# Kernel optimization log

Measured on AMD Instinct MI355X. Metric: run time of the kernel, lower is better.

## Reference

```python
import jax, jax.numpy as jnp
import numpy as np

ALPHA = 0.2  # LeakyReLU negative slope
N, F_IN, F_OUT = 8192, 512, 64
NEG_BIG = -9e15


def setup_inputs() -> dict:
    key = jax.random.key(0)
    k1, k2, k3, k4 = jax.random.split(key, 4)
    h = jax.random.normal(k1, (N, F_IN), dtype=jnp.float32)
    # xavier_uniform with gain 1.414
    lim_w = 1.414 * np.sqrt(6.0 / (F_IN + F_OUT))
    W = jax.random.uniform(k2, (F_IN, F_OUT), dtype=jnp.float32, minval=-lim_w, maxval=lim_w)
    lim_a = 1.414 * np.sqrt(6.0 / (2 * F_OUT + 1))
    a = jax.random.uniform(k3, (2 * F_OUT, 1), dtype=jnp.float32, minval=-lim_a, maxval=lim_a)
    adj = jax.random.randint(k4, (N, N), 0, 2, dtype=jnp.int32)
    return {"h": h, "W": W, "a": a, "adj": adj}


def reference(h, W, a, adj):
    Wh = h @ W                                  # [N, F_OUT]
    f_out = Wh.shape[1]
    a1 = a[:f_out, 0]                            # source half of attention vector
    a2 = a[f_out:, 0]                            # target half
    # e_ij = LeakyReLU(Wh_i . a1 + Wh_j . a2); equals cat([Wh_i, Wh_j]) @ a
    e = jax.nn.leaky_relu(jnp.matmul(Wh, a1)[:, None] + jnp.matmul(Wh, a2)[None, :], ALPHA)  # [N, N]
    attention = jnp.where(adj > 0, e, NEG_BIG)
    attention = jax.nn.softmax(attention, axis=1)
    # dropout is a no-op at inference (training=False)
    h_prime = attention @ Wh                     # [N, F_OUT]
    return jax.nn.elu(h_prime)                   # concat=True -> ELU
```

## Files before the change

### kernel.cpp

```cpp
#include <hip/hip_runtime.h>
#include <hip/hip_bf16.h>


typedef _Float16 f16;
typedef _Float16 f16x8 __attribute__((ext_vector_type(8)));
typedef float f32x4 __attribute__((ext_vector_type(4)));

#define GAT_N 8192
#define GAT_FIN 512
#define GAT_FOUT 64
#define GAT_ALPHA 0.2f

__global__ void k0_wtrans(const float* __restrict__ W, f16* __restrict__ WT) {
    int idx = blockIdx.x * blockDim.x + threadIdx.x;
    int k = idx >> 6, c = idx & 63;
    WT[c * GAT_FIN + k] = (f16)W[idx];
}

__global__ __launch_bounds__(64) void k1_gemm(const float* __restrict__ h,
        const f16* __restrict__ WT, const float* __restrict__ a,
        f16* __restrict__ WhT, float* __restrict__ s1, float* __restrict__ s2) {
    int lane = threadIdx.x & 63;
    int l15 = lane & 15, quad = lane >> 4;
    int rb = blockIdx.x * 16;
    size_t arow = (size_t)(rb + l15) * GAT_FIN;

    f32x4 acc[4] = {};
    for (int k0 = 0; k0 < GAT_FIN; k0 += 32) {
        int kb = k0 + quad * 8;
        const float4* hp = (const float4*)(h + arow + kb);
        float4 h0 = hp[0], h1 = hp[1];
        f16x8 af = { (f16)h0.x, (f16)h0.y, (f16)h0.z, (f16)h0.w,
                     (f16)h1.x, (f16)h1.y, (f16)h1.z, (f16)h1.w };
#pragma unroll
        for (int t = 0; t < 4; t++) {
            f16x8 bf = *(const f16x8*)(WT + (t * 16 + l15) * GAT_FIN + kb);
            acc[t] = __builtin_amdgcn_mfma_f32_16x16x32_f16(af, bf, acc[t], 0, 0, 0);
        }
    }

    float a1v[4], a2v[4];
#pragma unroll
    for (int t = 0; t < 4; t++) {
        a1v[t] = a[t * 16 + l15];
        a2v[t] = a[GAT_FOUT + t * 16 + l15];
    }
#pragma unroll
    for (int reg = 0; reg < 4; reg++) {
        int r = rb + quad * 4 + reg;
        float p1 = 0.f, p2 = 0.f;
#pragma unroll
        for (int t = 0; t < 4; t++) {
            float v = acc[t][reg];
            WhT[(size_t)(t * 16 + l15) * GAT_N + r] = (f16)v;
            p1 += v * a1v[t];
            p2 += v * a2v[t];
        }
#pragma unroll
        for (int off = 1; off < 16; off <<= 1) {
            p1 += __shfl_xor(p1, off);
            p2 += __shfl_xor(p2, off);
        }
        if (l15 == 0) { s1[r] = p1; s2[r] = p2; }
    }
}

__global__ void k2_max(const float* __restrict__ s2, float* __restrict__ mx) {
    __shared__ float red[256];
    float m = -1e30f;
    for (int i = threadIdx.x; i < GAT_N; i += 256) m = fmaxf(m, s2[i]);
    red[threadIdx.x] = m;
    __syncthreads();
    for (int s = 128; s > 0; s >>= 1) {
        if (threadIdx.x < s) red[threadIdx.x] = fmaxf(red[threadIdx.x], red[threadIdx.x + s]);
        __syncthreads();
    }
    if (threadIdx.x == 0) mx[0] = red[0];
}

__global__ __launch_bounds__(512) void k3_attn(const int* __restrict__ adj,
        const f16* __restrict__ WhT, const float* __restrict__ s1,
        const float* __restrict__ s2, const float* __restrict__ mxp,
        float* __restrict__ out) {
    __shared__ float accbuf[8][16][64];
    __shared__ float dbuf[8][16];

    int tid = threadIdx.x;
    int w = tid >> 6, lane = tid & 63;
    int l15 = lane & 15, quad = lane >> 4;
    int rb = blockIdx.x * 16;
    int row = rb + l15;

    float s1r = s1[row];
    float cr = s1r + mxp[0];
    cr = fmaxf(cr, GAT_ALPHA * cr);

    f32x4 acc[4] = {};
    float dacc = 0.f;
    const int* adjrow = adj + (size_t)row * GAT_N;

    for (int step = w; step < GAT_N / 32; step += 8) {
        int kb = step * 32 + quad * 8;
        int4 av0 = *(const int4*)(adjrow + kb);
        int4 av1 = *(const int4*)(adjrow + kb + 4);
        float4 sv0 = *(const float4*)(s2 + kb);
        float4 sv1 = *(const float4*)(s2 + kb + 4);

        int   am[8] = { av0.x, av0.y, av0.z, av0.w, av1.x, av1.y, av1.z, av1.w };
        float sv[8] = { sv0.x, sv0.y, sv0.z, sv0.w, sv1.x, sv1.y, sv1.z, sv1.w };

        f16x8 af;
#pragma unroll
        for (int j = 0; j < 8; j++) {
            float e = s1r + sv[j];
            e = fmaxf(e, GAT_ALPHA * e);
            float pf = __expf(e - cr);
            pf = (am[j] > 0) ? pf : 0.0f;
            dacc += pf;
            af[j] = (f16)pf;
        }
#pragma unroll
        for (int t = 0; t < 4; t++) {
            f16x8 bf = *(const f16x8*)(WhT + (size_t)(t * 16 + l15) * GAT_N + kb);
            acc[t] = __builtin_amdgcn_mfma_f32_16x16x32_f16(af, bf, acc[t], 0, 0, 0);
        }
    }

    dacc += __shfl_xor(dacc, 16);
    dacc += __shfl_xor(dacc, 32);

#pragma unroll
    for (int t = 0; t < 4; t++)
#pragma unroll
        for (int reg = 0; reg < 4; reg++)
            accbuf[w][quad * 4 + reg][t * 16 + l15] = acc[t][reg];
    if (quad == 0) dbuf[w][l15] = dacc;
    __syncthreads();

    for (int o = tid; o < 16 * 64; o += 512) {
        int r = o >> 6, c = o & 63;
        float num = 0.f, den = 0.f;
#pragma unroll
        for (int ww = 0; ww < 8; ww++) { num += accbuf[ww][r][c]; den += dbuf[ww][r]; }
        float hp = num / den;
        out[(size_t)(rb + r) * GAT_FOUT + c] = hp > 0.f ? hp : expm1f(hp);
    }
}

extern "C" void kernel_launch(void* const* d_in, const int* in_sizes, int n_in,
                              void* d_out, int out_size, void* d_ws, size_t ws_size,
                              hipStream_t stream) {
    const float* h   = (const float*)d_in[0];
    const float* W   = (const float*)d_in[1];
    const float* a   = (const float*)d_in[2];
    const int*   adj = (const int*)d_in[3];
    float* out = (float*)d_out;

    char* ws = (char*)d_ws;
    f16*   WT  = (f16*)ws;
    f16*   WhT = (f16*)(ws + 65536);
    float* s1  = (float*)(ws + 65536 + 1048576);
    float* s2  = (float*)(ws + 65536 + 1048576 + 32768);
    float* mx  = (float*)(ws + 65536 + 1048576 + 65536);

    k0_wtrans<<<128, 256, 0, stream>>>(W, WT);
    k1_gemm<<<512, 64, 0, stream>>>(h, WT, a, WhT, s1, s2);
    k2_max<<<1, 256, 0, stream>>>(s2, mx);
    k3_attn<<<512, 512, 0, stream>>>(adj, WhT, s1, s2, mx, out);
}
```

Before: 433.2 us.

## Coalesce adj row reads and stage softmax weights through double-buffered LDS

The attention kernel now assigns whole adjacency rows to half-waves, so each lane reads contiguous 16-byte chunks along a row instead of scattered 32-byte pieces across 16 rows. The exp and mask results are written into a double-buffered shared-memory tile in MFMA A-operand layout, then read back by each wave for the MFMA accumulation. Loads for the next 512-column chunk are issued before the current chunk's MFMAs to overlap the memory latency. This adds an LDS round trip and a block-wide barrier per chunk, and sets a minimum-blocks occupancy hint.

```diff
diff --git a/kernel.cpp b/kernel.cpp
--- a/kernel.cpp
+++ b/kernel.cpp
@@ -3,6 +3,7 @@
 
 
 typedef _Float16 f16;
+typedef _Float16 f16x2 __attribute__((ext_vector_type(2)));
 typedef _Float16 f16x8 __attribute__((ext_vector_type(8)));
 typedef float f32x4 __attribute__((ext_vector_type(4)));
 
@@ -78,72 +79,105 @@
     if (threadIdx.x == 0) mx[0] = red[0];
 }
 
-__global__ __launch_bounds__(512) void k3_attn(const int* __restrict__ adj,
+__global__ __launch_bounds__(512, 4) void k3_attn(const int* __restrict__ adj,
         const f16* __restrict__ WhT, const float* __restrict__ s1,
         const float* __restrict__ s2, const float* __restrict__ mxp,
         float* __restrict__ out) {
-    __shared__ float accbuf[8][16][64];
-    __shared__ float dbuf[8][16];
+    __shared__ __align__(16) char smem[2 * 16 * 520 * 2];
+    f16* pbuf = (f16*)smem;
+    float (*accbuf)[16][64] = (float (*)[16][64])smem;
+    __shared__ float dbuf2[16];
 
     int tid = threadIdx.x;
     int w = tid >> 6, lane = tid & 63;
     int l15 = lane & 15, quad = lane >> 4;
+    int hhalf = lane >> 5, q = lane & 31;
     int rb = blockIdx.x * 16;
-    int row = rb + l15;
-
-    float s1r = s1[row];
+    int r = 2 * w + hhalf;
+
+    float s1r = s1[rb + r];
     float cr = s1r + mxp[0];
     cr = fmaxf(cr, GAT_ALPHA * cr);
-
+    const int* adjrow = adj + (size_t)(rb + r) * GAT_N;
+
+    float dacc = 0.f;
     f32x4 acc[4] = {};
-    float dacc = 0.f;
-    const int* adjrow = adj + (size_t)row * GAT_N;
-
-    for (int step = w; step < GAT_N / 32; step += 8) {
-        int kb = step * 32 + quad * 8;
-        int4 av0 = *(const int4*)(adjrow + kb);
-        int4 av1 = *(const int4*)(adjrow + kb + 4);
-        float4 sv0 = *(const float4*)(s2 + kb);
-        float4 sv1 = *(const float4*)(s2 + kb + 4);
-
-        int   am[8] = { av0.x, av0.y, av0.z, av0.w, av1.x, av1.y, av1.z, av1.w };
-        float sv[8] = { sv0.x, sv0.y, sv0.z, sv0.w, sv1.x, sv1.y, sv1.z, sv1.w };
-
-        f16x8 af;
-#pragma unroll
-        for (int j = 0; j < 8; j++) {
-            float e = s1r + sv[j];
-            e = fmaxf(e, GAT_ALPHA * e);
-            float pf = __expf(e - cr);
-            pf = (am[j] > 0) ? pf : 0.0f;
-            dacc += pf;
-            af[j] = (f16)pf;
-        }
-#pragma unroll
-        for (int t = 0; t < 4; t++) {
-            f16x8 bf = *(const f16x8*)(WhT + (size_t)(t * 16 + l15) * GAT_N + kb);
-            acc[t] = __builtin_amdgcn_mfma_f32_16x16x32_f16(af, bf, acc[t], 0, 0, 0);
-        }
-    }
-
-    dacc += __shfl_xor(dacc, 16);
-    dacc += __shfl_xor(dacc, 32);
+    int4   av[4];
+    float4 sv[4];
+
+    auto stage = [&](int bb) {
+#pragma unroll
+        for (int p = 0; p < 4; p++) {
+            int   am[4]  = { av[p].x, av[p].y, av[p].z, av[p].w };
+            float svv[4] = { sv[p].x, sv[p].y, sv[p].z, sv[p].w };
+            int base = (4 * p + (q >> 3)) * 520 + ((q >> 1) & 3) * 128 + r * 8 + (q & 1) * 4;
+            f16 pf[4];
+#pragma unroll
+            for (int j = 0; j < 4; j++) {
+                float e = s1r + svv[j];
+                e = fmaxf(e, GAT_ALPHA * e);
+                float pv = __expf(e - cr);
+                pv = (am[j] > 0) ? pv : 0.0f;
+                dacc += pv;
+                pf[j] = (f16)pv;
+            }
+            f16x2 lo = { pf[0], pf[1] }, hi = { pf[2], pf[3] };
+            *(f16x2*)&pbuf[bb * 8320 + base]     = lo;
+            *(f16x2*)&pbuf[bb * 8320 + base + 2] = hi;
+        }
+    };
+
+#pragma unroll
+    for (int p = 0; p < 4; p++) {
+        int c0 = p * 128 + q * 4;
+        av[p] = *(const int4*)(adjrow + c0);
+        sv[p] = *(const float4*)(s2 + c0);
+    }
+    stage(0);
+    __syncthreads();
+
+    for (int rd = 0; rd < 16; rd++) {
+        int b = rd & 1;
+        if (rd < 15) {
+#pragma unroll
+            for (int p = 0; p < 4; p++) {
+                int c0 = (rd + 1) * 512 + p * 128 + q * 4;
+                av[p] = *(const int4*)(adjrow + c0);
+                sv[p] = *(const float4*)(s2 + c0);
+            }
+        }
+#pragma unroll
+        for (int sl = 0; sl < 2; sl++) {
+            int s_loc = 2 * w + sl;
+            f16x8 af = *(const f16x8*)&pbuf[b * 8320 + s_loc * 520 + lane * 8];
+            int kb = rd * 512 + s_loc * 32 + quad * 8;
+#pragma unroll
+            for (int t = 0; t < 4; t++) {
+                f16x8 bf = *(const f16x8*)(WhT + (size_t)(t * 16 + l15) * GAT_N + kb);
+                acc[t] = __builtin_amdgcn_mfma_f32_16x16x32_f16(af, bf, acc[t], 0, 0, 0);
+            }
+        }
+        if (rd < 15) stage(1 - b);
+        __syncthreads();
+    }
 
 #pragma unroll
     for (int t = 0; t < 4; t++)
 #pragma unroll
         for (int reg = 0; reg < 4; reg++)
             accbuf[w][quad * 4 + reg][t * 16 + l15] = acc[t][reg];
-    if (quad == 0) dbuf[w][l15] = dacc;
+#pragma unroll
+    for (int off = 16; off >= 1; off >>= 1) dacc += __shfl_xor(dacc, off);
+    if (q == 0) dbuf2[r] = dacc;
     __syncthreads();
 
     for (int o = tid; o < 16 * 64; o += 512) {
-        int r = o >> 6, c = o & 63;
-        float num = 0.f, den = 0.f;
-#pragma unroll
-        for (int ww = 0; ww < 8; ww++) { num += accbuf[ww][r][c]; den += dbuf[ww][r]; }
-        float hp = num / den;
-        out[(size_t)(rb + r) * GAT_FOUT + c] = hp > 0.f ? hp : expm1f(hp);
+        int rr = o >> 6, c = o & 63;
+        float num = 0.f;
+#pragma unroll
+        for (int ww = 0; ww < 8; ww++) num += accbuf[ww][rr][c];
+        float hp = num / dbuf2[rr];
+        out[(size_t)(rb + rr) * GAT_FOUT + c] = hp > 0.f ? hp : expm1f(hp);
     }
 }
 
```

After: 409.8 us. 5.4% less time.
